# Kernel tuning notes

Hardware: AMD Instinct MI355X
Metric: run time of the kernel (lower is better)

Reference implementation:

```python
import jax, jax.numpy as jnp
import numpy as np

H = 8        # num_heads
D = 768      # d_model
DH = D // H  # d_head = 96


def setup_inputs() -> dict:
    key = jax.random.key(0)
    ks = jax.random.split(key, 12)
    B, S = 4, 2048
    s_in = 1.0 / np.sqrt(D)
    s_cat = 1.0 / np.sqrt(D)
    return {
        "input_querys": jax.random.normal(ks[0], (B, S, D), jnp.float32),
        "input_key": jax.random.normal(ks[1], (B, S, D), jnp.float32),
        "input_values": jax.random.normal(ks[2], (B, S, D), jnp.float32),
        # per-head projection weights, stacked over the head axis
        "Wq": jax.random.normal(ks[3], (H, D, DH), jnp.float32) * s_in,
        "bq": jax.random.normal(ks[4], (H, DH), jnp.float32) * s_in,
        "Wk": jax.random.normal(ks[5], (H, D, DH), jnp.float32) * s_in,
        "bk": jax.random.normal(ks[6], (H, DH), jnp.float32) * s_in,
        "Wv": jax.random.normal(ks[7], (H, D, DH), jnp.float32) * s_in,
        "bv": jax.random.normal(ks[8], (H, DH), jnp.float32) * s_in,
        # output linear: (H*DH) -> D
        "Wo": jax.random.normal(ks[9], (H * DH, D), jnp.float32) * s_cat,
        "bo": jax.random.normal(ks[10], (D,), jnp.float32) * s_cat,
    }


def reference(input_querys, input_key, input_values, Wq, bq, Wk, bk, Wv, bv, Wo, bo):
    # Per-head linear projections (vectorized over the head axis)
    # q/k/v: [B,S,D] -> [B,H,S,DH]
    Q = jnp.einsum("bsd,hdk->bhsk", input_querys, Wq) + bq[None, :, None, :]
    K = jnp.einsum("bsd,hdk->bhsk", input_key, Wk) + bk[None, :, None, :]
    V = jnp.einsum("bsd,hdk->bhsk", input_values, Wv) + bv[None, :, None, :]

    scale = 1.0 / jnp.sqrt(jnp.asarray(DH, Q.dtype))
    scores = jnp.einsum("bhsk,bhtk->bhst", Q, K) * scale  # [B,H,S,S]
    attn = jax.nn.softmax(scores, axis=-1)
    out = jnp.einsum("bhst,bhtk->bhsk", attn, V)  # [B,H,S,DH]

    # concat heads (head-major order matches torch.cat over ModuleList)
    B, _, S, _ = out.shape
    cat = out.transpose(0, 2, 1, 3).reshape(B, S, H * DH)
    return cat @ Wo + bo
```

## Files before the change

### kernel.cpp

```cpp
#include <hip/hip_runtime.h>


typedef unsigned short u16;
typedef _Float16 h16;
typedef h16 h16x8 __attribute__((ext_vector_type(8)));
typedef __fp16 fp16x2 __attribute__((ext_vector_type(2)));
typedef unsigned short u16x8 __attribute__((ext_vector_type(8)));
typedef unsigned short u16x4 __attribute__((ext_vector_type(4)));
typedef float f32x4 __attribute__((ext_vector_type(4)));

__device__ __forceinline__ u16 f2h(float f) {
  union { h16 h; u16 u; } c; c.h = (h16)f; return c.u;
}

__device__ __forceinline__ void gll16(const void* g, void* l) {
  __builtin_amdgcn_global_load_lds(
      (const __attribute__((address_space(1))) void*)g,
      (__attribute__((address_space(3))) void*)l, 16, 0, 0);
}

__global__ __launch_bounds__(256) void prep_kernel(
    const float* __restrict__ Wq, const float* __restrict__ Wk,
    const float* __restrict__ Wv, const float* __restrict__ Wo,
    u16* __restrict__ WqT, u16* __restrict__ WkT,
    u16* __restrict__ WvT, u16* __restrict__ WoT)
{
  int idx = (blockIdx.x * 256 + threadIdx.x) * 8;
  int region = idx / 589824;
  int i = idx % 589824;
  int n = i / 768;
  int d = i % 768;
  u16x8 v;
  if (region == 3) {
    #pragma unroll
    for (int j = 0; j < 8; j++) v[j] = f2h(Wo[(size_t)(d + j) * 768 + n]);
    *(u16x8*)(&WoT[i]) = v;
  } else {
    int h = n / 96, kk = n % 96;
    const float* W = (region == 0) ? Wq : (region == 1) ? Wk : Wv;
    u16* T = (region == 0) ? WqT : (region == 1) ? WkT : WvT;
    #pragma unroll
    for (int j = 0; j < 8; j++) v[j] = f2h(W[(size_t)h * 73728 + (size_t)(d + j) * 96 + kk]);
    *(u16x8*)(&T[i]) = v;
  }
}

#define GK 768

__global__ __launch_bounds__(256) void gemm_qkv(
    const float* __restrict__ Xq, const float* __restrict__ Xk,
    const float* __restrict__ Xv, const u16* __restrict__ WT,
    const float* __restrict__ bq, const float* __restrict__ bk,
    const float* __restrict__ bv,
    u16* __restrict__ Q16, u16* __restrict__ K16, u16* __restrict__ VT)
{
  const int z = blockIdx.z;
  const float* A = (z == 0) ? Xq : (z == 1) ? Xk : Xv;
  const u16* BT = WT + (size_t)z * 589824;
  const float* bias = (z == 0) ? bq : (z == 1) ? bk : bv;

  __shared__ __align__(16) u16 As[128 * 32];
  __shared__ __align__(16) u16 Bs[64 * 32];
  const int tid = threadIdx.x;
  const int wave = tid >> 6;
  const int lane = tid & 63;
  const int quad = lane >> 4;
  const int l16 = lane & 15;
  const int m0 = blockIdx.x * 128;
  const int n0 = blockIdx.y * 64;

  f32x4 acc[2][4];
  #pragma unroll
  for (int i = 0; i < 2; i++)
    #pragma unroll
    for (int j = 0; j < 4; j++) acc[i][j] = (f32x4){0.f, 0.f, 0.f, 0.f};

  const int ar = tid >> 2;
  const int ac = (tid & 3) * 8;

  f32x4 pf[4];
  u16x8 pb;
  {
    pf[0] = *(const f32x4*)(&A[(size_t)(m0 + ar) * GK + ac]);
    pf[1] = *(const f32x4*)(&A[(size_t)(m0 + ar) * GK + ac + 4]);
    pf[2] = *(const f32x4*)(&A[(size_t)(m0 + 64 + ar) * GK + ac]);
    pf[3] = *(const f32x4*)(&A[(size_t)(m0 + 64 + ar) * GK + ac + 4]);
    pb = *(const u16x8*)(&BT[(size_t)(n0 + ar) * GK + ac]);
  }

  for (int kt = 0; kt < 24; kt++) {
    u16x8 h0, h1;
    #pragma unroll
    for (int j = 0; j < 4; j++) {
      h0[j] = f2h(pf[0][j]); h0[4 + j] = f2h(pf[1][j]);
      h1[j] = f2h(pf[2][j]); h1[4 + j] = f2h(pf[3][j]);
    }
    *(u16x8*)(&As[ar * 32 + ac]) = h0;
    *(u16x8*)(&As[(64 + ar) * 32 + ac]) = h1;
    *(u16x8*)(&Bs[ar * 32 + ac]) = pb;
    __syncthreads();

    if (kt + 1 < 24) {
      const int k0 = (kt + 1) * 32;
      pf[0] = *(const f32x4*)(&A[(size_t)(m0 + ar) * GK + k0 + ac]);
      pf[1] = *(const f32x4*)(&A[(size_t)(m0 + ar) * GK + k0 + ac + 4]);
      pf[2] = *(const f32x4*)(&A[(size_t)(m0 + 64 + ar) * GK + k0 + ac]);
      pf[3] = *(const f32x4*)(&A[(size_t)(m0 + 64 + ar) * GK + k0 + ac + 4]);
      pb = *(const u16x8*)(&BT[(size_t)(n0 + ar) * GK + k0 + ac]);
    }

    h16x8 af[2], bf[4];
    #pragma unroll
    for (int mf = 0; mf < 2; mf++)
      af[mf] = *(const h16x8*)(&As[(wave * 32 + mf * 16 + l16) * 32 + quad * 8]);
    #pragma unroll
    for (int nf = 0; nf < 4; nf++)
      bf[nf] = *(const h16x8*)(&Bs[(nf * 16 + l16) * 32 + quad * 8]);
    #pragma unroll
    for (int mf = 0; mf < 2; mf++)
      #pragma unroll
      for (int nf = 0; nf < 4; nf++)
        acc[mf][nf] = __builtin_amdgcn_mfma_f32_16x16x32_f16(af[mf], bf[nf], acc[mf][nf], 0, 0, 0);

    if (kt + 1 < 24) __syncthreads();
  }

  u16* Yr = (z == 0) ? Q16 : K16;
  #pragma unroll
  for (int nf = 0; nf < 4; nf++) {
    const int n = n0 + nf * 16 + l16;
    const float bv2 = bias[n];
    #pragma unroll
    for (int mf = 0; mf < 2; mf++) {
      const int m = m0 + wave * 32 + mf * 16 + quad * 4;
      if (z == 2) {
        const int b = m >> 11, s = m & 2047;
        u16x4 pk;
        #pragma unroll
        for (int r = 0; r < 4; r++) pk[r] = f2h(acc[mf][nf][r] + bv2);
        *(u16x4*)(&VT[(size_t)b * 768 * 2048 + (size_t)n * 2048 + s]) = pk;
      } else {
        #pragma unroll
        for (int r = 0; r < 4; r++)
          Yr[(size_t)(m + r) * GK + n] = f2h(acc[mf][nf][r] + bv2);
      }
    }
  }
}

__global__ __launch_bounds__(256) void gemm_o(
    const u16* __restrict__ A, const u16* __restrict__ BT,
    const float* __restrict__ bias, float* __restrict__ Y)
{
  __shared__ __align__(16) u16 As[128 * 32];
  __shared__ __align__(16) u16 Bs[64 * 32];
  const int tid = threadIdx.x;
  const int wave = tid >> 6;
  const int lane = tid & 63;
  const int quad = lane >> 4;
  const int l16 = lane & 15;
  const int m0 = blockIdx.x * 128;
  const int n0 = blockIdx.y * 64;

  f32x4 acc[2][4];
  #pragma unroll
  for (int i = 0; i < 2; i++)
    #pragma unroll
    for (int j = 0; j < 4; j++) acc[i][j] = (f32x4){0.f, 0.f, 0.f, 0.f};

  const int Lr = lane >> 2, Lc = (lane & 3) * 8;
  const u16* gA0 = A + (size_t)(m0 + wave * 32 + Lr) * GK + Lc;
  const u16* gA1 = gA0 + (size_t)16 * GK;
  const u16* gB  = BT + (size_t)(n0 + wave * 16 + Lr) * GK + Lc;
  u16* lA0 = &As[(wave * 32) * 32];
  u16* lA1 = &As[(wave * 32 + 16) * 32];
  u16* lB  = &Bs[(wave * 16) * 32];

  for (int kt = 0; kt < 24; kt++) {
    gll16(gA0, lA0);
    gll16(gA1, lA1);
    gll16(gB, lB);
    gA0 += 32; gA1 += 32; gB += 32;
    __syncthreads();

    h16x8 af[2], bf[4];
    #pragma unroll
    for (int mf = 0; mf < 2; mf++)
      af[mf] = *(const h16x8*)(&As[(wave * 32 + mf * 16 + l16) * 32 + quad * 8]);
    #pragma unroll
    for (int nf = 0; nf < 4; nf++)
      bf[nf] = *(const h16x8*)(&Bs[(nf * 16 + l16) * 32 + quad * 8]);
    #pragma unroll
    for (int mf = 0; mf < 2; mf++)
      #pragma unroll
      for (int nf = 0; nf < 4; nf++)
        acc[mf][nf] = __builtin_amdgcn_mfma_f32_16x16x32_f16(af[mf], bf[nf], acc[mf][nf], 0, 0, 0);
    __syncthreads();
  }

  #pragma unroll
  for (int nf = 0; nf < 4; nf++) {
    const int n = n0 + nf * 16 + l16;
    const float bv = bias[n];
    #pragma unroll
    for (int mf = 0; mf < 2; mf++) {
      const int m = m0 + wave * 32 + mf * 16 + quad * 4;
      #pragma unroll
      for (int r = 0; r < 4; r++)
        Y[(size_t)(m + r) * GK + n] = acc[mf][nf][r] + bv;
    }
  }
}

#define SEQ 2048
#define LQK 104
#define LVT 72
#define LPS 72

__global__ __launch_bounds__(512, 4) void attn_kernel(
    const u16* __restrict__ Q, const u16* __restrict__ K,
    const u16* __restrict__ VT, u16* __restrict__ O)
{
  __shared__ __align__(16) u16 Ks[64 * LQK];
  __shared__ __align__(16) u16 Vt[96 * LVT];
  __shared__ __align__(16) u16 Ps[8][16 * LPS];

  const int tid = threadIdx.x;
  const int wave = tid >> 6;
  const int lane = tid & 63;
  const int quad = lane >> 4;
  const int l16 = lane & 15;

  const int bh = blockIdx.y;
  const int b = bh >> 3, h = bh & 7;
  const int q0 = blockIdx.x * 128;

  const size_t batch_off = (size_t)b * SEQ * 768;
  const u16* Kg = K + batch_off + h * 96;
  const u16* Vg = VT + (size_t)b * 768 * 2048 + (size_t)(h * 96) * 2048;

  h16x8 qf[3];
  {
    const u16* Qrow = Q + batch_off + (size_t)(q0 + wave * 16 + l16) * 768 + h * 96 + quad * 8;
    #pragma unroll
    for (int ks = 0; ks < 3; ks++) qf[ks] = *(const h16x8*)(&Qrow[ks * 32]);
  }

  const int kr0 = tid / 12, kc0 = (tid % 12) * 8;
  const int kr1 = (tid + 512) / 12, kc1 = ((tid + 512) % 12) * 8;
  const int vr0 = tid >> 3, vc0 = (tid & 7) * 8;
  const int vr1 = (tid + 512) >> 3, vc1 = ((tid + 512) & 7) * 8;
  const bool extra = tid < 256;

  f32x4 o[6];
  #pragma unroll
  for (int i = 0; i < 6; i++) o[i] = (f32x4){0.f, 0.f, 0.f, 0.f};
  float m_raw = -1e30f, lrow = 0.f;
  const float sc = 0.14724498f;

  u16* Pw = &Ps[wave][0];

  u16x8 kA, kB, vA, vB;
  kA = *(const u16x8*)(&Kg[(size_t)kr0 * 768 + kc0]);
  vA = *(const u16x8*)(&Vg[(size_t)vr0 * 2048 + vc0]);
  if (extra) {
    kB = *(const u16x8*)(&Kg[(size_t)kr1 * 768 + kc1]);
    vB = *(const u16x8*)(&Vg[(size_t)vr1 * 2048 + vc1]);
  }

  for (int kt = 0; kt < SEQ / 64; kt++) {
    *(u16x8*)(&Ks[kr0 * LQK + kc0]) = kA;
    *(u16x8*)(&Vt[vr0 * LVT + vc0]) = vA;
    if (extra) {
      *(u16x8*)(&Ks[kr1 * LQK + kc1]) = kB;
      *(u16x8*)(&Vt[vr1 * LVT + vc1]) = vB;
    }
    __syncthreads();

    if (kt + 1 < SEQ / 64) {
      const u16* Kn = Kg + (size_t)(kt + 1) * 64 * 768;
      const u16* Vn = Vg + (size_t)(kt + 1) * 64;
      kA = *(const u16x8*)(&Kn[(size_t)kr0 * 768 + kc0]);
      vA = *(const u16x8*)(&Vn[(size_t)vr0 * 2048 + vc0]);
      if (extra) {
        kB = *(const u16x8*)(&Kn[(size_t)kr1 * 768 + kc1]);
        vB = *(const u16x8*)(&Vn[(size_t)vr1 * 2048 + vc1]);
      }
    }

    f32x4 s[4];
    #pragma unroll
    for (int kf = 0; kf < 4; kf++) s[kf] = (f32x4){0.f, 0.f, 0.f, 0.f};
    #pragma unroll
    for (int ks = 0; ks < 3; ks++) {
      #pragma unroll
      for (int kf = 0; kf < 4; kf++) {
        h16x8 a = *(const h16x8*)(&Ks[(kf * 16 + l16) * LQK + ks * 32 + quad * 8]);
        s[kf] = __builtin_amdgcn_mfma_f32_16x16x32_f16(a, qf[ks], s[kf], 0, 0, 0);
      }
    }

    float mx = s[0][0];
    #pragma unroll
    for (int kf = 0; kf < 4; kf++)
      #pragma unroll
      for (int r = 0; r < 4; r++) mx = fmaxf(mx, s[kf][r]);
    mx = fmaxf(mx, __shfl_xor(mx, 16));
    mx = fmaxf(mx, __shfl_xor(mx, 32));
    const float mold = m_raw;
    m_raw = fmaxf(mold, mx);
    const float c0 = sc * m_raw;
    float ps = 0.f;
    #pragma unroll
    for (int kf = 0; kf < 4; kf++)
      #pragma unroll
      for (int r = 0; r < 4; r++) {
        float p = exp2f(fmaf(s[kf][r], sc, -c0));
        s[kf][r] = p;
        ps += p;
      }
    if (__any(m_raw > mold)) {
      const float alpha = exp2f(sc * (mold - m_raw));
      lrow *= alpha;
      #pragma unroll
      for (int nfo = 0; nfo < 6; nfo++)
        #pragma unroll
        for (int r = 0; r < 4; r++) o[nfo][r] *= alpha;
    }
    lrow += ps;

    #pragma unroll
    for (int kf = 0; kf < 4; kf++)
      #pragma unroll
      for (int rp = 0; rp < 4; rp += 2) {
        fp16x2 pk = __builtin_amdgcn_cvt_pkrtz(s[kf][rp], s[kf][rp + 1]);
        *(fp16x2*)(&Pw[l16 * LPS + kf * 16 + quad * 4 + rp]) = pk;
      }

    #pragma unroll
    for (int ks = 0; ks < 2; ks++) {
      h16x8 pfr = *(const h16x8*)(&Pw[l16 * LPS + ks * 32 + quad * 8]);
      #pragma unroll
      for (int nfo = 0; nfo < 6; nfo++) {
        h16x8 vfr = *(const h16x8*)(&Vt[(nfo * 16 + l16) * LVT + ks * 32 + quad * 8]);
        o[nfo] = __builtin_amdgcn_mfma_f32_16x16x32_f16(vfr, pfr, o[nfo], 0, 0, 0);
      }
    }
    __syncthreads();
  }

  lrow += __shfl_xor(lrow, 16);
  lrow += __shfl_xor(lrow, 32);
  const float inv = 1.0f / lrow;
  u16* Ob = O + batch_off + (size_t)(q0 + wave * 16 + l16) * 768 + h * 96;
  #pragma unroll
  for (int nfo = 0; nfo < 6; nfo++) {
    fp16x2 lo = __builtin_amdgcn_cvt_pkrtz(o[nfo][0] * inv, o[nfo][1] * inv);
    fp16x2 hi = __builtin_amdgcn_cvt_pkrtz(o[nfo][2] * inv, o[nfo][3] * inv);
    *(fp16x2*)(&Ob[nfo * 16 + quad * 4]) = lo;
    *(fp16x2*)(&Ob[nfo * 16 + quad * 4 + 2]) = hi;
  }
}

extern "C" void kernel_launch(void* const* d_in, const int* in_sizes, int n_in,
                              void* d_out, int out_size, void* d_ws, size_t ws_size,
                              hipStream_t stream) {
  const float* Xq = (const float*)d_in[0];
  const float* Xk = (const float*)d_in[1];
  const float* Xv = (const float*)d_in[2];
  const float* Wq = (const float*)d_in[3];
  const float* bq = (const float*)d_in[4];
  const float* Wk = (const float*)d_in[5];
  const float* bk = (const float*)d_in[6];
  const float* Wv = (const float*)d_in[7];
  const float* bv = (const float*)d_in[8];
  const float* Wo = (const float*)d_in[9];
  const float* bo = (const float*)d_in[10];

  u16* wsu = (u16*)d_ws;
  u16* WT  = wsu;
  u16* WoT = wsu + 3 * 589824;
  u16* Q16 = wsu + 4 * 589824;

  u16* outu = (u16*)d_out;
  u16* VTb = outu;
  u16* K16 = outu + 6291456;

  u16* A16 = (u16*)d_in[0];

  prep_kernel<<<1152, 256, 0, stream>>>(Wq, Wk, Wv, Wo, WT, WT + 589824, WT + 2 * 589824, WoT);
  gemm_qkv<<<dim3(64, 12, 3), 256, 0, stream>>>(Xq, Xk, Xv, WT, bq, bk, bv, Q16, K16, VTb);
  attn_kernel<<<dim3(16, 32), 512, 0, stream>>>(Q16, K16, VTb, A16);
  gemm_o<<<dim3(64, 12), 256, 0, stream>>>(A16, WoT, bo, (float*)d_out);
}
```

Before: 313.0 us.

## Pre-convert K/V inputs to fp16, use direct LDS loads, lazy softmax rescale

The prep kernel now also converts the key and value activations to fp16 in workspace. For the K and V projections, the QKV GEMM then streams those tiles straight into LDS with global_load_lds instead of loading fp32 into registers and converting, though this path has no register prefetch of the next tile. The attention kernel raises wave priority around its MFMA blocks. It also rescales the running max only when the new max exceeds the old by a threshold, which skips most rescale work but lets exponentials grow up to a bounded factor, risking fp16 overflow in P. The extra conversion pass adds a full read and write of the K/V inputs.

Result: faster. 299.9 us (-4.2%).

```diff
diff --git a/kernel.cpp b/kernel.cpp
--- a/kernel.cpp
+++ b/kernel.cpp
@@ -22,10 +22,27 @@
 __global__ __launch_bounds__(256) void prep_kernel(
     const float* __restrict__ Wq, const float* __restrict__ Wk,
     const float* __restrict__ Wv, const float* __restrict__ Wo,
+    const float* __restrict__ Xk, const float* __restrict__ Xv,
     u16* __restrict__ WqT, u16* __restrict__ WkT,
-    u16* __restrict__ WvT, u16* __restrict__ WoT)
+    u16* __restrict__ WvT, u16* __restrict__ WoT,
+    u16* __restrict__ Xk16, u16* __restrict__ Xv16)
 {
-  int idx = (blockIdx.x * 256 + threadIdx.x) * 8;
+  const long gid = (long)blockIdx.x * 256 + threadIdx.x;
+  if (gid >= 294912) {
+    long i = gid - 294912;
+    const int t = (i >= 786432) ? 1 : 0;
+    const long e = (i - (long)t * 786432) * 8;
+    const float* src = t ? Xv : Xk;
+    u16* dst = t ? Xv16 : Xk16;
+    f32x4 a = *(const f32x4*)(&src[e]);
+    f32x4 b = *(const f32x4*)(&src[e + 4]);
+    u16x8 v;
+    #pragma unroll
+    for (int j = 0; j < 4; j++) { v[j] = f2h(a[j]); v[4 + j] = f2h(b[j]); }
+    *(u16x8*)(&dst[e]) = v;
+    return;
+  }
+  int idx = (int)gid * 8;
   int region = idx / 589824;
   int i = idx % 589824;
   int n = i / 768;
@@ -48,14 +65,13 @@
 #define GK 768
 
 __global__ __launch_bounds__(256) void gemm_qkv(
-    const float* __restrict__ Xq, const float* __restrict__ Xk,
-    const float* __restrict__ Xv, const u16* __restrict__ WT,
+    const float* __restrict__ Xq, const u16* __restrict__ Xk16,
+    const u16* __restrict__ Xv16, const u16* __restrict__ WT,
     const float* __restrict__ bq, const float* __restrict__ bk,
     const float* __restrict__ bv,
     u16* __restrict__ Q16, u16* __restrict__ K16, u16* __restrict__ VT)
 {
   const int z = blockIdx.z;
-  const float* A = (z == 0) ? Xq : (z == 1) ? Xk : Xv;
   const u16* BT = WT + (size_t)z * 589824;
   const float* bias = (z == 0) ? bq : (z == 1) ? bk : bv;
 
@@ -75,54 +91,88 @@
     #pragma unroll
     for (int j = 0; j < 4; j++) acc[i][j] = (f32x4){0.f, 0.f, 0.f, 0.f};
 
-  const int ar = tid >> 2;
-  const int ac = (tid & 3) * 8;
-
-  f32x4 pf[4];
-  u16x8 pb;
-  {
-    pf[0] = *(const f32x4*)(&A[(size_t)(m0 + ar) * GK + ac]);
-    pf[1] = *(const f32x4*)(&A[(size_t)(m0 + ar) * GK + ac + 4]);
-    pf[2] = *(const f32x4*)(&A[(size_t)(m0 + 64 + ar) * GK + ac]);
-    pf[3] = *(const f32x4*)(&A[(size_t)(m0 + 64 + ar) * GK + ac + 4]);
-    pb = *(const u16x8*)(&BT[(size_t)(n0 + ar) * GK + ac]);
-  }
-
-  for (int kt = 0; kt < 24; kt++) {
-    u16x8 h0, h1;
-    #pragma unroll
-    for (int j = 0; j < 4; j++) {
-      h0[j] = f2h(pf[0][j]); h0[4 + j] = f2h(pf[1][j]);
-      h1[j] = f2h(pf[2][j]); h1[4 + j] = f2h(pf[3][j]);
-    }
-    *(u16x8*)(&As[ar * 32 + ac]) = h0;
-    *(u16x8*)(&As[(64 + ar) * 32 + ac]) = h1;
-    *(u16x8*)(&Bs[ar * 32 + ac]) = pb;
-    __syncthreads();
-
-    if (kt + 1 < 24) {
-      const int k0 = (kt + 1) * 32;
-      pf[0] = *(const f32x4*)(&A[(size_t)(m0 + ar) * GK + k0 + ac]);
-      pf[1] = *(const f32x4*)(&A[(size_t)(m0 + ar) * GK + k0 + ac + 4]);
-      pf[2] = *(const f32x4*)(&A[(size_t)(m0 + 64 + ar) * GK + k0 + ac]);
-      pf[3] = *(const f32x4*)(&A[(size_t)(m0 + 64 + ar) * GK + k0 + ac + 4]);
-      pb = *(const u16x8*)(&BT[(size_t)(n0 + ar) * GK + k0 + ac]);
-    }
-
-    h16x8 af[2], bf[4];
-    #pragma unroll
-    for (int mf = 0; mf < 2; mf++)
-      af[mf] = *(const h16x8*)(&As[(wave * 32 + mf * 16 + l16) * 32 + quad * 8]);
-    #pragma unroll
-    for (int nf = 0; nf < 4; nf++)
-      bf[nf] = *(const h16x8*)(&Bs[(nf * 16 + l16) * 32 + quad * 8]);
-    #pragma unroll
-    for (int mf = 0; mf < 2; mf++)
+  if (z == 0) {
+    const float* A = Xq;
+    const int ar = tid >> 2;
+    const int ac = (tid & 3) * 8;
+
+    f32x4 pf[4];
+    u16x8 pb;
+    {
+      pf[0] = *(const f32x4*)(&A[(size_t)(m0 + ar) * GK + ac]);
+      pf[1] = *(const f32x4*)(&A[(size_t)(m0 + ar) * GK + ac + 4]);
+      pf[2] = *(const f32x4*)(&A[(size_t)(m0 + 64 + ar) * GK + ac]);
+      pf[3] = *(const f32x4*)(&A[(size_t)(m0 + 64 + ar) * GK + ac + 4]);
+      pb = *(const u16x8*)(&BT[(size_t)(n0 + ar) * GK + ac]);
+    }
+
+    for (int kt = 0; kt < 24; kt++) {
+      u16x8 h0, h1;
+      #pragma unroll
+      for (int j = 0; j < 4; j++) {
+        h0[j] = f2h(pf[0][j]); h0[4 + j] = f2h(pf[1][j]);
+        h1[j] = f2h(pf[2][j]); h1[4 + j] = f2h(pf[3][j]);
+      }
+      *(u16x8*)(&As[ar * 32 + ac]) = h0;
+      *(u16x8*)(&As[(64 + ar) * 32 + ac]) = h1;
+      *(u16x8*)(&Bs[ar * 32 + ac]) = pb;
+      __syncthreads();
+
+      if (kt + 1 < 24) {
+        const int k0 = (kt + 1) * 32;
+        pf[0] = *(const f32x4*)(&A[(size_t)(m0 + ar) * GK + k0 + ac]);
+        pf[1] = *(const f32x4*)(&A[(size_t)(m0 + ar) * GK + k0 + ac + 4]);
+        pf[2] = *(const f32x4*)(&A[(size_t)(m0 + 64 + ar) * GK + k0 + ac]);
+        pf[3] = *(const f32x4*)(&A[(size_t)(m0 + 64 + ar) * GK + k0 + ac + 4]);
+        pb = *(const u16x8*)(&BT[(size_t)(n0 + ar) * GK + k0 + ac]);
+      }
+
+      h16x8 af[2], bf[4];
+      #pragma unroll
+      for (int mf = 0; mf < 2; mf++)
+        af[mf] = *(const h16x8*)(&As[(wave * 32 + mf * 16 + l16) * 32 + quad * 8]);
       #pragma unroll
       for (int nf = 0; nf < 4; nf++)
-        acc[mf][nf] = __builtin_amdgcn_mfma_f32_16x16x32_f16(af[mf], bf[nf], acc[mf][nf], 0, 0, 0);
-
-    if (kt + 1 < 24) __syncthreads();
+        bf[nf] = *(const h16x8*)(&Bs[(nf * 16 + l16) * 32 + quad * 8]);
+      #pragma unroll
+      for (int mf = 0; mf < 2; mf++)
+        #pragma unroll
+        for (int nf = 0; nf < 4; nf++)
+          acc[mf][nf] = __builtin_amdgcn_mfma_f32_16x16x32_f16(af[mf], bf[nf], acc[mf][nf], 0, 0, 0);
+
+      if (kt + 1 < 24) __syncthreads();
+    }
+  } else {
+    const u16* A = (z == 1) ? Xk16 : Xv16;
+    const int Lr = lane >> 2, Lc = (lane & 3) * 8;
+    const u16* gA0 = A + (size_t)(m0 + wave * 32 + Lr) * GK + Lc;
+    const u16* gA1 = gA0 + (size_t)16 * GK;
+    const u16* gB  = BT + (size_t)(n0 + wave * 16 + Lr) * GK + Lc;
+    u16* lA0 = &As[(wave * 32) * 32];
+    u16* lA1 = &As[(wave * 32 + 16) * 32];
+    u16* lB  = &Bs[(wave * 16) * 32];
+
+    for (int kt = 0; kt < 24; kt++) {
+      gll16(gA0, lA0);
+      gll16(gA1, lA1);
+      gll16(gB, lB);
+      gA0 += 32; gA1 += 32; gB += 32;
+      __syncthreads();
+
+      h16x8 af[2], bf[4];
+      #pragma unroll
+      for (int mf = 0; mf < 2; mf++)
+        af[mf] = *(const h16x8*)(&As[(wave * 32 + mf * 16 + l16) * 32 + quad * 8]);
+      #pragma unroll
+      for (int nf = 0; nf < 4; nf++)
+        bf[nf] = *(const h16x8*)(&Bs[(nf * 16 + l16) * 32 + quad * 8]);
+      #pragma unroll
+      for (int mf = 0; mf < 2; mf++)
+        #pragma unroll
+        for (int nf = 0; nf < 4; nf++)
+          acc[mf][nf] = __builtin_amdgcn_mfma_f32_16x16x32_f16(af[mf], bf[nf], acc[mf][nf], 0, 0, 0);
+      __syncthreads();
+    }
   }
 
   u16* Yr = (z == 0) ? Q16 : K16;
@@ -291,6 +341,7 @@
     f32x4 s[4];
     #pragma unroll
     for (int kf = 0; kf < 4; kf++) s[kf] = (f32x4){0.f, 0.f, 0.f, 0.f};
+    __builtin_amdgcn_s_setprio(1);
     #pragma unroll
     for (int ks = 0; ks < 3; ks++) {
       #pragma unroll
@@ -299,6 +350,7 @@
         s[kf] = __builtin_amdgcn_mfma_f32_16x16x32_f16(a, qf[ks], s[kf], 0, 0, 0);
       }
     }
+    __builtin_amdgcn_s_setprio(0);
 
     float mx = s[0][0];
     #pragma unroll
@@ -307,8 +359,16 @@
       for (int r = 0; r < 4; r++) mx = fmaxf(mx, s[kf][r]);
     mx = fmaxf(mx, __shfl_xor(mx, 16));
     mx = fmaxf(mx, __shfl_xor(mx, 32));
-    const float mold = m_raw;
-    m_raw = fmaxf(mold, mx);
+    if (__any(mx > m_raw + 54.0f)) {
+      const float mnew = fmaxf(m_raw, mx);
+      const float alpha = exp2f(sc * (m_raw - mnew));
+      lrow *= alpha;
+      #pragma unroll
+      for (int nfo = 0; nfo < 6; nfo++)
+        #pragma unroll
+        for (int r = 0; r < 4; r++) o[nfo][r] *= alpha;
+      m_raw = mnew;
+    }
     const float c0 = sc * m_raw;
     float ps = 0.f;
     #pragma unroll
@@ -319,14 +379,6 @@
         s[kf][r] = p;
         ps += p;
       }
-    if (__any(m_raw > mold)) {
-      const float alpha = exp2f(sc * (mold - m_raw));
-      lrow *= alpha;
-      #pragma unroll
-      for (int nfo = 0; nfo < 6; nfo++)
-        #pragma unroll
-        for (int r = 0; r < 4; r++) o[nfo][r] *= alpha;
-    }
     lrow += ps;
 
     #pragma unroll
@@ -337,6 +389,7 @@
         *(fp16x2*)(&Pw[l16 * LPS + kf * 16 + quad * 4 + rp]) = pk;
       }
 
+    __builtin_amdgcn_s_setprio(1);
     #pragma unroll
     for (int ks = 0; ks < 2; ks++) {
       h16x8 pfr = *(const h16x8*)(&Pw[l16 * LPS + ks * 32 + quad * 8]);
@@ -346,6 +399,7 @@
         o[nfo] = __builtin_amdgcn_mfma_f32_16x16x32_f16(vfr, pfr, o[nfo], 0, 0, 0);
       }
     }
+    __builtin_amdgcn_s_setprio(0);
     __syncthreads();
   }
 
@@ -378,9 +432,11 @@
   const float* bo = (const float*)d_in[10];
 
   u16* wsu = (u16*)d_ws;
-  u16* WT  = wsu;
-  u16* WoT = wsu + 3 * 589824;
-  u16* Q16 = wsu + 4 * 589824;
+  u16* WT   = wsu;
+  u16* WoT  = wsu + 3 * 589824;
+  u16* Q16  = wsu + 4 * 589824;
+  u16* Xk16 = Q16 + 6291456;
+  u16* Xv16 = Xk16 + 6291456;
 
   u16* outu = (u16*)d_out;
   u16* VTb = outu;
@@ -388,8 +444,10 @@
 
   u16* A16 = (u16*)d_in[0];
 
-  prep_kernel<<<1152, 256, 0, stream>>>(Wq, Wk, Wv, Wo, WT, WT + 589824, WT + 2 * 589824, WoT);
-  gemm_qkv<<<dim3(64, 12, 3), 256, 0, stream>>>(Xq, Xk, Xv, WT, bq, bk, bv, Q16, K16, VTb);
+  prep_kernel<<<7296, 256, 0, stream>>>(Wq, Wk, Wv, Wo, Xk, Xv,
+                                        WT, WT + 589824, WT + 2 * 589824, WoT,
+                                        Xk16, Xv16);
+  gemm_qkv<<<dim3(64, 12, 3), 256, 0, stream>>>(Xq, Xk16, Xv16, WT, bq, bk, bv, Q16, K16, VTb);
   attn_kernel<<<dim3(16, 32), 512, 0, stream>>>(Q16, K16, VTb, A16);
   gemm_o<<<dim3(64, 12), 256, 0, stream>>>(A16, WoT, bo, (float*)d_out);
 }
```
